# Optimization experiments

Measured on AMD Instinct MI355X. Metric: run time of the kernel, lower is better.

## Reference

```python
import jax, jax.numpy as jnp
import numpy as np

N = 8192
M = 16
F_NODE = 128
HID = 512


def setup_inputs() -> dict:
    key = jax.random.key(0)
    ks = jax.random.split(key, 10)
    node_in_fea = jax.random.normal(ks[0], (N, F_NODE), dtype=jnp.float32)
    edge_fea_idx = jax.random.randint(ks[1], (N, M), 0, N, dtype=jnp.int64)
    s_emb = 1.0 / np.sqrt(F_NODE)
    s_h = 1.0 / np.sqrt(HID)
    W_emb = jax.random.uniform(ks[2], (F_NODE, HID), jnp.float32, -s_emb, s_emb)
    b_emb = jax.random.uniform(ks[3], (HID,), jnp.float32, -s_emb, s_emb)
    W1 = jax.random.uniform(ks[4], (HID, HID), jnp.float32, -s_h, s_h)
    b1 = jax.random.uniform(ks[5], (HID,), jnp.float32, -s_h, s_h)
    W2 = jax.random.uniform(ks[6], (HID, HID), jnp.float32, -s_h, s_h)
    b2 = jax.random.uniform(ks[7], (HID,), jnp.float32, -s_h, s_h)
    W3 = jax.random.uniform(ks[8], (HID, HID), jnp.float32, -s_h, s_h)
    b3 = jax.random.uniform(ks[9], (HID,), jnp.float32, -s_h, s_h)
    return {"node_in_fea": node_in_fea, "edge_fea_idx": edge_fea_idx,
            "W_emb": W_emb, "b_emb": b_emb, "W1": W1, "b1": b1,
            "W2": W2, "b2": b2, "W3": W3, "b3": b3}


def _normalized_adj(edge_fea_idx, n):
    # build dense adjacency: adj[i, j] += 1 for each valid neighbor j of i
    rows = jnp.broadcast_to(jnp.arange(n)[:, None], edge_fea_idx.shape)
    valid = edge_fea_idx >= 0  # -1 marks invalid neighbor
    cols = jnp.where(valid, edge_fea_idx, 0)
    vals = valid.astype(jnp.float32)
    adj = jnp.zeros((n, n), jnp.float32).at[rows.reshape(-1), cols.reshape(-1)].add(vals.reshape(-1))
    # add self-loops, symmetric normalization D^{-1/2} A D^{-1/2}
    adj = adj + jnp.eye(n, dtype=jnp.float32)
    deg = jnp.sum(adj, axis=1)
    d_inv_sqrt = jnp.where(deg > 0, deg ** -0.5, 0.0)
    return adj * d_inv_sqrt[:, None] * d_inv_sqrt[None, :]


def reference(node_in_fea, edge_fea_idx, W_emb, b_emb, W1, b1, W2, b2, W3, b3):
    adj = _normalized_adj(edge_fea_idx, node_in_fea.shape[0])
    x = node_in_fea @ W_emb + b_emb          # (N, HID)
    x = jax.nn.relu((adj @ x) @ W1 + b1)     # gcn1 + relu
    x = jax.nn.relu((adj @ x) @ W2 + b2)     # gcn2 + relu
    x = (adj @ x) @ W3 + b3                  # gcn3 (no relu)
    return x
```

## Files before the change

### kernel.cpp

```cpp
#include <hip/hip_runtime.h>
#include <stdint.h>

#define NN 8192
#define MM 16
#define FN 128
#define HH 512

typedef unsigned short u16;
typedef unsigned int u32;
typedef __bf16 bf16;
typedef __bf16 bf16x8 __attribute__((ext_vector_type(8)));
typedef float f32x4 __attribute__((ext_vector_type(4)));

__device__ __forceinline__ void gld_lds16(const u16* g, u16* l) {
  __builtin_amdgcn_global_load_lds(
      (const __attribute__((address_space(1))) void*)g,
      (__attribute__((address_space(3))) void*)l, 16, 0, 0);
}

__device__ __forceinline__ int probe_f32(const u16* w) {
  int lane = threadIdx.x & 63;
  int e = (w[2 * lane] >> 7) & 0xFF;
  unsigned long long m = __ballot(!(e == 0 || (e >= 90 && e <= 140)));
  return __popcll(m) >= 8;
}
__device__ __forceinline__ int probe_i64(const u32* w) {
  int lane = threadIdx.x & 63;
  unsigned long long m = __ballot(lane < 32 && w[2 * lane + 1] != 0);
  return m == 0;
}

__device__ __forceinline__ bf16 cvt_elem(const void* p, size_t i, int f32) {
  return f32 ? (bf16)((const float*)p)[i] : ((const bf16*)p)[i];
}

__device__ __forceinline__ void transpose_tile(const void* __restrict__ W,
                                               u16* __restrict__ T, int tt,
                                               int f32in, u16* sm) {
  const int k0 = (tt >> 4) * 32, n0 = (tt & 15) * 32;
  const int tx = threadIdx.x & 31, ty = threadIdx.x >> 5;
#pragma unroll
  for (int r = ty; r < 32; r += 8) {
    bf16 v = cvt_elem(W, (size_t)(k0 + r) * HH + n0 + tx, f32in);
    sm[r * 33 + tx] = *(u16*)&v;
  }
  __syncthreads();
#pragma unroll
  for (int r = ty; r < 32; r += 8)
    T[(size_t)(n0 + r) * HH + k0 + tx] = sm[tx * 33 + r];
}

__global__ __launch_bounds__(256) void prep1_kernel(
    const u16* __restrict__ node, const u32* __restrict__ idxw,
    const void* __restrict__ Wemb, const void* __restrict__ W1,
    const void* __restrict__ W2, const void* __restrict__ W3,
    float* __restrict__ dis, u16* __restrict__ TW1, u16* __restrict__ TW2,
    u16* __restrict__ TW3, u16* __restrict__ WembB) {
  __shared__ u16 sm[32 * 33];
  const int bid = blockIdx.x, tid = threadIdx.x;
  if (bid < 768) {
    const int f32in = probe_f32(node);
    const int q = bid >> 8, tt = bid & 255;
    transpose_tile(q == 0 ? W1 : q == 1 ? W2 : W3,
                   q == 0 ? TW1 : q == 1 ? TW2 : TW3, tt, f32in, sm);
  } else if (bid < 800) {
    const int i64 = probe_i64(idxw);
    const int* idx = (const int*)idxw;
    const int i = (bid - 768) * 256 + tid;
    int c = 1;
#pragma unroll
    for (int e = 0; e < MM; ++e) c += (idx[(i * MM + e) << i64] >= 0) ? 1 : 0;
    dis[i] = rsqrtf((float)c);
  } else {
    const int f32in = probe_f32(node);
    const size_t g = ((size_t)(bid - 800) * 256 + tid) * 8;
    bf16x8 o;
    if (f32in) {
      f32x4 a = *(const f32x4*)&((const float*)Wemb)[g];
      f32x4 b = *(const f32x4*)&((const float*)Wemb)[g + 4];
#pragma unroll
      for (int t = 0; t < 4; ++t) { o[t] = (bf16)a[t]; o[4 + t] = (bf16)b[t]; }
    } else {
      o = *(const bf16x8*)&((const u16*)Wemb)[g];
    }
    *(bf16x8*)&WembB[g] = o;
  }
}

__device__ __forceinline__ void gemm_tile(const void* __restrict__ A, int K,
                                          int af32, const u16* __restrict__ Bt,
                                          const float* __restrict__ biasf,
                                          int rtile, int ctile,
                                          u16* __restrict__ C, int cstride,
                                          u16* As, u16* Bs) {
  const int tid = threadIdx.x;
  const int wave = tid >> 6, lane = tid & 63;
  const int wr = wave >> 1, wc = wave & 1;
  const int quad = lane >> 4, l16 = lane & 15;
  f32x4 acc[2][4] = {};

  int arow[2], agc[2], brow[4], bgc[4];
#pragma unroll
  for (int i = 0; i < 2; ++i) {
    int c = i * 256 + tid;
    arow[i] = c >> 3;
    agc[i] = (c & 7) ^ (arow[i] & 7);
  }
#pragma unroll
  for (int i = 0; i < 4; ++i) {
    int c = i * 256 + tid;
    brow[i] = c >> 3;
    bgc[i] = (c & 7) ^ (brow[i] & 7);
  }
  u16* AsW = As + wave * 512;
  u16* BsW = Bs + wave * 512;

  for (int k0 = 0; k0 < K; k0 += 64) {
    __syncthreads();
    if (af32) {
      const float* Af = (const float*)A;
      bf16x8 v[2];
#pragma unroll
      for (int i = 0; i < 2; ++i) {
        const float* p = &Af[(size_t)(rtile * 64 + arow[i]) * K + k0 + agc[i] * 8];
        f32x4 x0 = *(const f32x4*)p, x1 = *(const f32x4*)(p + 4);
#pragma unroll
        for (int t = 0; t < 4; ++t) {
          v[i][t] = (bf16)x0[t];
          v[i][4 + t] = (bf16)x1[t];
        }
      }
#pragma unroll
      for (int i = 0; i < 2; ++i) *(bf16x8*)&As[(i * 256 + tid) * 8] = v[i];
    } else {
      const u16* Ab = (const u16*)A;
#pragma unroll
      for (int i = 0; i < 2; ++i)
        gld_lds16(&Ab[(size_t)(rtile * 64 + arow[i]) * K + k0 + agc[i] * 8],
                  AsW + i * 2048);
    }
#pragma unroll
    for (int i = 0; i < 4; ++i)
      gld_lds16(&Bt[(size_t)(ctile * 128 + brow[i]) * K + k0 + bgc[i] * 8],
                BsW + i * 2048);
    __syncthreads();
#pragma unroll
    for (int h = 0; h < 2; ++h) {
      bf16x8 af[2], bfr[4];
#pragma unroll
      for (int i = 0; i < 2; ++i) {
        int r = wr * 32 + i * 16 + l16;
        int cc = (h * 4 + quad) ^ (r & 7);
        af[i] = *(const bf16x8*)&As[r * 64 + cc * 8];
      }
#pragma unroll
      for (int j = 0; j < 4; ++j) {
        int n = wc * 64 + j * 16 + l16;
        int cc = (h * 4 + quad) ^ (n & 7);
        bfr[j] = *(const bf16x8*)&Bs[n * 64 + cc * 8];
      }
#pragma unroll
      for (int i = 0; i < 2; ++i)
#pragma unroll
        for (int j = 0; j < 4; ++j)
          acc[i][j] = __builtin_amdgcn_mfma_f32_16x16x32_bf16(af[i], bfr[j],
                                                              acc[i][j], 0, 0, 0);
    }
  }

  const int crow0 = rtile * 64 + wr * 32 + quad * 4;
  const int ccol0 = ctile * 128 + wc * 64 + l16;
#pragma unroll
  for (int j = 0; j < 4; ++j) {
    const int col = ccol0 + j * 16;
    const float bv = biasf ? biasf[col] : 0.f;
#pragma unroll
    for (int i = 0; i < 2; ++i)
#pragma unroll
      for (int r = 0; r < 4; ++r) {
        bf16 o = (bf16)(acc[i][j][r] + bv);
        C[(size_t)(crow0 + i * 16 + r) * cstride + col] = *(u16*)&o;
      }
  }
}

__global__ __launch_bounds__(256) void prep2_kernel(
    const u16* __restrict__ node, const void* __restrict__ bemb,
    const u16* __restrict__ TW1, const u16* __restrict__ WembB,
    const void* __restrict__ Wemb, u16* __restrict__ TWc,
    float* __restrict__ bvec) {
  __shared__ __align__(16) u16 As[64 * 64];
  __shared__ __align__(16) u16 Bs[128 * 64];
  __shared__ float bembS[HH];
  const int bid = blockIdx.x, tid = threadIdx.x;
  const int f32in = probe_f32(node);
  if (bid < 8) {
    const u16* Bt = f32in ? WembB : (const u16*)Wemb;
    gemm_tile(TW1, HH, 0, Bt, nullptr, bid, 0, TWc, FN, As, Bs);
  } else {
    bembS[tid] = (float)cvt_elem(bemb, tid, f32in);
    bembS[256 + tid] = (float)cvt_elem(bemb, 256 + tid, f32in);
    __syncthreads();
    const int n = (bid - 8) * 256 + tid;
    float acc = 0.f;
#pragma unroll 8
    for (int m = 0; m < HH; m += 8) {
      bf16x8 w = *(const bf16x8*)&TW1[(size_t)n * HH + m];
#pragma unroll
      for (int j = 0; j < 8; ++j) acc += bembS[m + j] * (float)w[j];
    }
    bvec[n] = acc;
  }
}

__global__ __launch_bounds__(256) void g1_kernel(const u16* __restrict__ node,
                                                 const u16* __restrict__ TWc,
                                                 const float* __restrict__ bvec,
                                                 u16* __restrict__ C) {
  __shared__ __align__(16) u16 As[64 * 64];
  __shared__ __align__(16) u16 Bs[128 * 64];
  const int af32 = probe_f32(node);
  gemm_tile(node, FN, af32, TWc, bvec, blockIdx.x, blockIdx.y, C, HH, As, Bs);
}

__global__ __launch_bounds__(256) void gemm_mid(const u16* __restrict__ A,
                                                const u16* __restrict__ Bt,
                                                u16* __restrict__ C) {
  __shared__ __align__(16) u16 As[64 * 64];
  __shared__ __align__(16) u16 Bs[128 * 64];
  gemm_tile(A, HH, 0, Bt, nullptr, blockIdx.x, blockIdx.y, C, HH, As, Bs);
}

template <bool RELU, bool FINAL>
__global__ __launch_bounds__(256) void agg_kernel(
    const u16* __restrict__ t, const u32* __restrict__ idxw,
    const float* __restrict__ dis, const void* __restrict__ bias,
    const u16* __restrict__ nodeprobe, void* __restrict__ y) {
  const int i64 = probe_i64(idxw);
  const int f32io = probe_f32(nodeprobe);
  const int* idx = (const int*)idxw;
  const int b = blockIdx.x;
  const int strip = (b & 7) >> 1;
  const int grp = (b >> 3) * 2 + (b & 1);
  const int wave = threadIdx.x >> 6, lane = threadIdx.x & 63;
  const int node = grp * 16 + wave * 4 + (lane >> 4);
  const int c0 = strip * 128 + (lane & 15) * 8;
  const float wi = dis[node];
  float acc[8];
  bf16x8 xs = *(const bf16x8*)&t[(size_t)node * HH + c0];
#pragma unroll
  for (int k = 0; k < 8; ++k) acc[k] = wi * wi * (float)xs[k];
#pragma unroll
  for (int e = 0; e < MM; ++e) {
    const int j = idx[(node * MM + e) << i64];
    if (j >= 0) {
      const float w = wi * dis[j];
      bf16x8 v = *(const bf16x8*)&t[(size_t)j * HH + c0];
#pragma unroll
      for (int k = 0; k < 8; ++k) acc[k] += w * (float)v[k];
    }
  }
  float bv[8];
  if (f32io) {
    f32x4 b0 = *(const f32x4*)&((const float*)bias)[c0];
    f32x4 b1 = *(const f32x4*)&((const float*)bias)[c0 + 4];
#pragma unroll
    for (int k = 0; k < 4; ++k) { bv[k] = b0[k]; bv[4 + k] = b1[k]; }
  } else {
    bf16x8 bb = *(const bf16x8*)&((const u16*)bias)[c0];
#pragma unroll
    for (int k = 0; k < 8; ++k) bv[k] = (float)bb[k];
  }
#pragma unroll
  for (int k = 0; k < 8; ++k) {
    acc[k] += bv[k];
    if (RELU) acc[k] = fmaxf(acc[k], 0.f);
  }
  if (FINAL && f32io) {
    float* O = (float*)y;
    f32x4 o0, o1;
#pragma unroll
    for (int k = 0; k < 4; ++k) { o0[k] = acc[k]; o1[k] = acc[4 + k]; }
    *(f32x4*)&O[(size_t)node * HH + c0] = o0;
    *(f32x4*)&O[(size_t)node * HH + c0 + 4] = o1;
  } else {
    bf16x8 o;
#pragma unroll
    for (int k = 0; k < 8; ++k) o[k] = (bf16)acc[k];
    *(bf16x8*)&((u16*)y)[(size_t)node * HH + c0] = o;
  }
}

extern "C" void kernel_launch(void* const* d_in, const int* in_sizes, int n_in,
                              void* d_out, int out_size, void* d_ws, size_t ws_size,
                              hipStream_t stream) {
  const u16* node = (const u16*)d_in[0];
  const u32* idxw = (const u32*)d_in[1];
  const void* Wemb = d_in[2];
  const void* bemb = d_in[3];
  const void* W1 = d_in[4];
  const void* b1 = d_in[5];
  const void* W2 = d_in[6];
  const void* b2 = d_in[7];
  const void* W3 = d_in[8];
  const void* b3 = d_in[9];

  char* p = (char*)d_ws;
  float* dis = (float*)p;   p += NN * sizeof(float);
  float* bvec = (float*)p;  p += HH * sizeof(float);
  u16* TWc = (u16*)p;       p += (size_t)HH * FN * 2;
  u16* WembB = (u16*)p;     p += (size_t)FN * HH * 2;
  u16* TW1 = (u16*)p;       p += (size_t)HH * HH * 2;
  u16* TW2 = (u16*)p;       p += (size_t)HH * HH * 2;
  u16* TW3 = (u16*)p;       p += (size_t)HH * HH * 2;
  u16* xA = (u16*)p;
  u16* xO = (u16*)d_out;

  prep1_kernel<<<832, 256, 0, stream>>>(node, idxw, Wemb, W1, W2, W3, dis, TW1,
                                        TW2, TW3, WembB);
  prep2_kernel<<<10, 256, 0, stream>>>(node, bemb, TW1, WembB, Wemb, TWc, bvec);
  g1_kernel<<<dim3(128, 4), 256, 0, stream>>>(node, TWc, bvec, xA);
  agg_kernel<true, false>
      <<<NN / 4, 256, 0, stream>>>(xA, idxw, dis, b1, node, xO);
  gemm_mid<<<dim3(128, 4), 256, 0, stream>>>(xO, TW2, xA);
  agg_kernel<true, false>
      <<<NN / 4, 256, 0, stream>>>(xA, idxw, dis, b2, node, xO);
  gemm_mid<<<dim3(128, 4), 256, 0, stream>>>(xO, TW3, xA);
  agg_kernel<false, true>
      <<<NN / 4, 256, 0, stream>>>(xA, idxw, dis, b3, node, d_out);
}
```

Measured before the change: 165.3 us.

## Merge prep kernels, compute Wemb·W1 directly, defer W3 transpose into g1

The two prep kernels become one. The folded weight Wemb·W1 is now computed straight from the raw weights with on-the-fly conversion and a transposed store, so the W1 transpose and the Wemb bf16 copy are no longer needed. The W3 transpose moves into the g1 launch as extra blocks, and the bias projection reads W1 column-wise directly. This removes a kernel launch and a dependency stage, at the cost of strided scalar loads in the bias path and uncoalesced transposed stores in wc_tile.

```diff
diff --git a/kernel.cpp b/kernel.cpp
--- a/kernel.cpp
+++ b/kernel.cpp
@@ -29,7 +29,6 @@
   unsigned long long m = __ballot(lane < 32 && w[2 * lane + 1] != 0);
   return m == 0;
 }
-
 __device__ __forceinline__ bf16 cvt_elem(const void* p, size_t i, int f32) {
   return f32 ? (bf16)((const float*)p)[i] : ((const bf16*)p)[i];
 }
@@ -48,43 +47,6 @@
 #pragma unroll
   for (int r = ty; r < 32; r += 8)
     T[(size_t)(n0 + r) * HH + k0 + tx] = sm[tx * 33 + r];
-}
-
-__global__ __launch_bounds__(256) void prep1_kernel(
-    const u16* __restrict__ node, const u32* __restrict__ idxw,
-    const void* __restrict__ Wemb, const void* __restrict__ W1,
-    const void* __restrict__ W2, const void* __restrict__ W3,
-    float* __restrict__ dis, u16* __restrict__ TW1, u16* __restrict__ TW2,
-    u16* __restrict__ TW3, u16* __restrict__ WembB) {
-  __shared__ u16 sm[32 * 33];
-  const int bid = blockIdx.x, tid = threadIdx.x;
-  if (bid < 768) {
-    const int f32in = probe_f32(node);
-    const int q = bid >> 8, tt = bid & 255;
-    transpose_tile(q == 0 ? W1 : q == 1 ? W2 : W3,
-                   q == 0 ? TW1 : q == 1 ? TW2 : TW3, tt, f32in, sm);
-  } else if (bid < 800) {
-    const int i64 = probe_i64(idxw);
-    const int* idx = (const int*)idxw;
-    const int i = (bid - 768) * 256 + tid;
-    int c = 1;
-#pragma unroll
-    for (int e = 0; e < MM; ++e) c += (idx[(i * MM + e) << i64] >= 0) ? 1 : 0;
-    dis[i] = rsqrtf((float)c);
-  } else {
-    const int f32in = probe_f32(node);
-    const size_t g = ((size_t)(bid - 800) * 256 + tid) * 8;
-    bf16x8 o;
-    if (f32in) {
-      f32x4 a = *(const f32x4*)&((const float*)Wemb)[g];
-      f32x4 b = *(const f32x4*)&((const float*)Wemb)[g + 4];
-#pragma unroll
-      for (int t = 0; t < 4; ++t) { o[t] = (bf16)a[t]; o[4 + t] = (bf16)b[t]; }
-    } else {
-      o = *(const bf16x8*)&((const u16*)Wemb)[g];
-    }
-    *(bf16x8*)&WembB[g] = o;
-  }
 }
 
 __device__ __forceinline__ void gemm_tile(const void* __restrict__ A, int K,
@@ -184,51 +146,156 @@
   }
 }
 
-__global__ __launch_bounds__(256) void prep2_kernel(
-    const u16* __restrict__ node, const void* __restrict__ bemb,
-    const u16* __restrict__ TW1, const u16* __restrict__ WembB,
-    const void* __restrict__ Wemb, u16* __restrict__ TWc,
-    float* __restrict__ bvec) {
-  __shared__ __align__(16) u16 As[64 * 64];
-  __shared__ __align__(16) u16 Bs[128 * 64];
-  __shared__ float bembS[HH];
+__device__ void wc_tile(int vb, const void* __restrict__ Wemb,
+                        const void* __restrict__ W1, int f32in,
+                        u16* __restrict__ TWc, u16* As, u16* Bs) {
+  const int tid = threadIdx.x;
+  const int rtile = vb >> 2, ctile = vb & 3;
+  const int wave = tid >> 6, lane = tid & 63;
+  const int wr = wave >> 1, wc = wave & 1;
+  const int quad = lane >> 4, l16 = lane & 15;
+  f32x4 acc[2][4] = {};
+  int arow[2], agc[2];
+#pragma unroll
+  for (int i = 0; i < 2; ++i) {
+    int c = i * 256 + tid;
+    arow[i] = c >> 3;
+    agc[i] = (c & 7) ^ (arow[i] & 7);
+  }
+  for (int k0 = 0; k0 < HH; k0 += 64) {
+    __syncthreads();
+#pragma unroll
+    for (int i = 0; i < 2; ++i) {
+      size_t src = (size_t)(rtile * 64 + arow[i]) * HH + k0 + agc[i] * 8;
+      bf16x8 av;
+      if (f32in) {
+        const float* pp = (const float*)Wemb + src;
+        f32x4 x0 = *(const f32x4*)pp, x1 = *(const f32x4*)(pp + 4);
+#pragma unroll
+        for (int t = 0; t < 4; ++t) { av[t] = (bf16)x0[t]; av[4 + t] = (bf16)x1[t]; }
+      } else {
+        av = *(const bf16x8*)((const u16*)Wemb + src);
+      }
+      *(bf16x8*)&As[(i * 256 + tid) * 8] = av;
+    }
+#pragma unroll
+    for (int i = 0; i < 4; ++i) {
+      int t2 = i * 256 + tid;
+      int kk = t2 >> 4, seg = (t2 & 15) * 8;
+      size_t src = (size_t)(k0 + kk) * HH + ctile * 128 + seg;
+      bf16 e8[8];
+      if (f32in) {
+        const float* pp = (const float*)W1 + src;
+        f32x4 x0 = *(const f32x4*)pp, x1 = *(const f32x4*)(pp + 4);
+#pragma unroll
+        for (int t = 0; t < 4; ++t) { e8[t] = (bf16)x0[t]; e8[4 + t] = (bf16)x1[t]; }
+      } else {
+        bf16x8 v = *(const bf16x8*)((const u16*)W1 + src);
+#pragma unroll
+        for (int t = 0; t < 8; ++t) e8[t] = v[t];
+      }
+#pragma unroll
+      for (int j = 0; j < 8; ++j) {
+        int n = seg + j;
+        int cc = (kk >> 3) ^ j;
+        Bs[n * 64 + cc * 8 + (kk & 7)] = *(u16*)&e8[j];
+      }
+    }
+    __syncthreads();
+#pragma unroll
+    for (int h = 0; h < 2; ++h) {
+      bf16x8 af[2], bfr[4];
+#pragma unroll
+      for (int i = 0; i < 2; ++i) {
+        int r = wr * 32 + i * 16 + l16;
+        int cc = (h * 4 + quad) ^ (r & 7);
+        af[i] = *(const bf16x8*)&As[r * 64 + cc * 8];
+      }
+#pragma unroll
+      for (int j = 0; j < 4; ++j) {
+        int n = wc * 64 + j * 16 + l16;
+        int cc = (h * 4 + quad) ^ (n & 7);
+        bfr[j] = *(const bf16x8*)&Bs[n * 64 + cc * 8];
+      }
+#pragma unroll
+      for (int i = 0; i < 2; ++i)
+#pragma unroll
+        for (int j = 0; j < 4; ++j)
+          acc[i][j] = __builtin_amdgcn_mfma_f32_16x16x32_bf16(af[i], bfr[j],
+                                                              acc[i][j], 0, 0, 0);
+    }
+  }
+  const int crow0 = rtile * 64 + wr * 32 + quad * 4;
+  const int ccol0 = ctile * 128 + wc * 64 + l16;
+#pragma unroll
+  for (int j = 0; j < 4; ++j)
+#pragma unroll
+    for (int i = 0; i < 2; ++i)
+#pragma unroll
+      for (int r = 0; r < 4; ++r) {
+        bf16 o = (bf16)acc[i][j][r];
+        TWc[(size_t)(ccol0 + j * 16) * FN + crow0 + i * 16 + r] = *(u16*)&o;
+      }
+}
+
+__global__ __launch_bounds__(256) void prep_kernel(
+    const u16* __restrict__ node, const u32* __restrict__ idxw,
+    const void* __restrict__ Wemb, const void* __restrict__ bemb,
+    const void* __restrict__ W1, const void* __restrict__ W2,
+    float* __restrict__ dis, float* __restrict__ bvec, u16* __restrict__ TWc,
+    u16* __restrict__ TW2) {
+  __shared__ __align__(16) u16 smem[12288];
   const int bid = blockIdx.x, tid = threadIdx.x;
   const int f32in = probe_f32(node);
-  if (bid < 8) {
-    const u16* Bt = f32in ? WembB : (const u16*)Wemb;
-    gemm_tile(TW1, HH, 0, Bt, nullptr, bid, 0, TWc, FN, As, Bs);
+  if (bid < 256) {
+    transpose_tile(W2, TW2, bid, f32in, smem);
+  } else if (bid < 288) {
+    const int i64 = probe_i64(idxw);
+    const int* idx = (const int*)idxw;
+    const int i = (bid - 256) * 256 + tid;
+    int c = 1;
+#pragma unroll
+    for (int e = 0; e < MM; ++e) c += (idx[(i * MM + e) << i64] >= 0) ? 1 : 0;
+    dis[i] = rsqrtf((float)c);
+  } else if (bid < 296) {
+    wc_tile(bid - 288, Wemb, W1, f32in, TWc, smem, smem + 4096);
   } else {
+    float* bembS = (float*)smem;
     bembS[tid] = (float)cvt_elem(bemb, tid, f32in);
     bembS[256 + tid] = (float)cvt_elem(bemb, 256 + tid, f32in);
     __syncthreads();
-    const int n = (bid - 8) * 256 + tid;
+    const int n = (bid - 296) * 256 + tid;
     float acc = 0.f;
 #pragma unroll 8
-    for (int m = 0; m < HH; m += 8) {
-      bf16x8 w = *(const bf16x8*)&TW1[(size_t)n * HH + m];
-#pragma unroll
-      for (int j = 0; j < 8; ++j) acc += bembS[m + j] * (float)w[j];
-    }
+    for (int m = 0; m < HH; ++m)
+      acc += bembS[m] * (float)cvt_elem(W1, (size_t)m * HH + n, f32in);
     bvec[n] = acc;
   }
 }
 
 __global__ __launch_bounds__(256) void g1_kernel(const u16* __restrict__ node,
+                                                 const void* __restrict__ W3,
                                                  const u16* __restrict__ TWc,
                                                  const float* __restrict__ bvec,
+                                                 u16* __restrict__ TW3,
                                                  u16* __restrict__ C) {
-  __shared__ __align__(16) u16 As[64 * 64];
-  __shared__ __align__(16) u16 Bs[128 * 64];
-  const int af32 = probe_f32(node);
-  gemm_tile(node, FN, af32, TWc, bvec, blockIdx.x, blockIdx.y, C, HH, As, Bs);
+  __shared__ __align__(16) u16 smem[12288];
+  const int bid = blockIdx.x;
+  const int f32in = probe_f32(node);
+  if (bid < 512) {
+    gemm_tile(node, FN, f32in, TWc, bvec, bid >> 2, bid & 3, C, HH, smem,
+              smem + 4096);
+  } else {
+    transpose_tile(W3, TW3, bid - 512, f32in, smem);
+  }
 }
 
 __global__ __launch_bounds__(256) void gemm_mid(const u16* __restrict__ A,
                                                 const u16* __restrict__ Bt,
                                                 u16* __restrict__ C) {
-  __shared__ __align__(16) u16 As[64 * 64];
-  __shared__ __align__(16) u16 Bs[128 * 64];
-  gemm_tile(A, HH, 0, Bt, nullptr, blockIdx.x, blockIdx.y, C, HH, As, Bs);
+  __shared__ __align__(16) u16 smem[12288];
+  gemm_tile(A, HH, 0, Bt, nullptr, blockIdx.x, blockIdx.y, C, HH, smem,
+            smem + 4096);
 }
 
 template <bool RELU, bool FINAL>
@@ -309,17 +376,14 @@
   float* dis = (float*)p;   p += NN * sizeof(float);
   float* bvec = (float*)p;  p += HH * sizeof(float);
   u16* TWc = (u16*)p;       p += (size_t)HH * FN * 2;
-  u16* WembB = (u16*)p;     p += (size_t)FN * HH * 2;
-  u16* TW1 = (u16*)p;       p += (size_t)HH * HH * 2;
   u16* TW2 = (u16*)p;       p += (size_t)HH * HH * 2;
   u16* TW3 = (u16*)p;       p += (size_t)HH * HH * 2;
   u16* xA = (u16*)p;
   u16* xO = (u16*)d_out;
 
-  prep1_kernel<<<832, 256, 0, stream>>>(node, idxw, Wemb, W1, W2, W3, dis, TW1,
-                                        TW2, TW3, WembB);
-  prep2_kernel<<<10, 256, 0, stream>>>(node, bemb, TW1, WembB, Wemb, TWc, bvec);
-  g1_kernel<<<dim3(128, 4), 256, 0, stream>>>(node, TWc, bvec, xA);
+  prep_kernel<<<298, 256, 0, stream>>>(node, idxw, Wemb, bemb, W1, W2, dis,
+                                       bvec, TWc, TW2);
+  g1_kernel<<<768, 256, 0, stream>>>(node, W3, TWc, bvec, TW3, xA);
   agg_kernel<true, false>
       <<<NN / 4, 256, 0, stream>>>(xA, idxw, dis, b1, node, xO);
   gemm_mid<<<dim3(128, 4), 256, 0, stream>>>(xO, TW2, xA);
```

New measurement: 289.5 us. 75.1% more time.
